# Performance work log

Measured on AMD Instinct MI355X. Metric: run time of the kernel, lower is better.

## Reference

```python
import jax, jax.numpy as jnp
import numpy as np

HEADS = 16
LN_EPS = 1e-5


def setup_inputs() -> dict:
    key = jax.random.key(0)
    ks = jax.random.split(key, 4)
    B, S, C, U = 2, 2048, 1024, 1024
    scale = 1.0 / np.sqrt(C)
    return {
        "inputs": jax.random.normal(ks[0], (B, S, C), dtype=jnp.float32),
        "Wq": jax.random.normal(ks[1], (C, U), dtype=jnp.float32) * scale,
        "bq": jnp.zeros((U,), dtype=jnp.float32),
        "Wk": jax.random.normal(ks[2], (C, U), dtype=jnp.float32) * scale,
        "bk": jnp.zeros((U,), dtype=jnp.float32),
        "Wv": jax.random.normal(ks[3], (C, U), dtype=jnp.float32) * scale,
        "bv": jnp.zeros((U,), dtype=jnp.float32),
        "ln_gamma": jnp.ones((S, U), dtype=jnp.float32),
        "ln_beta": jnp.zeros((S, U), dtype=jnp.float32),
    }


def reference(inputs, Wq, bq, Wk, bk, Wv, bv, ln_gamma, ln_beta):
    B, S, C = inputs.shape
    U = Wq.shape[1]
    H = HEADS
    dh = U // H

    Q = inputs @ Wq + bq  # [B,S,U]
    K = inputs @ Wk + bk
    V = inputs @ Wv + bv

    # torch: concat(split(X, U//H, dim=-1), dim=0) -> head-major stacking on batch
    def split_heads(X):
        return jnp.moveaxis(X.reshape(B, S, H, dh), 2, 0).reshape(H * B, S, dh)

    Q_, K_, V_ = split_heads(Q), split_heads(K), split_heads(V)

    scores = jnp.einsum('bqd,bkd->bqk', Q_, K_) / jnp.sqrt(jnp.float32(dh))
    tri = jnp.tril(jnp.ones((S, S), dtype=bool))  # causal mask
    scores = jnp.where(tri[None, :, :], scores, jnp.float32(-1e9))
    attn = jax.nn.softmax(scores, axis=-1)
    out_ = jnp.einsum('bqk,bkd->bqd', attn, V_)  # [H*B,S,dh]

    # inverse: split on batch into H chunks of size B, concat on feature dim
    out = jnp.moveaxis(out_.reshape(H, B, S, dh), 0, 2).reshape(B, S, U)

    out = out + inputs  # residual

    # LayerNorm over normalized_shape=[S, U] (joint seq+feature stats)
    mu = jnp.mean(out, axis=(-2, -1), keepdims=True)
    var = jnp.mean(jnp.square(out - mu), axis=(-2, -1), keepdims=True)
    out = (out - mu) / jnp.sqrt(var + LN_EPS) * ln_gamma + ln_beta
    return out
```

## Files before the change

### kernel.cpp

```cpp
#include <hip/hip_runtime.h>
#include <hip/hip_bf16.h>


typedef __bf16 bf16_t;
typedef __bf16 bf16x8 __attribute__((ext_vector_type(8)));
typedef __bf16 bf16x4 __attribute__((ext_vector_type(4)));
typedef _Float16 f16_t;
typedef _Float16 f16x2 __attribute__((ext_vector_type(2)));
typedef _Float16 f16x4 __attribute__((ext_vector_type(4)));
typedef _Float16 f16x8 __attribute__((ext_vector_type(8)));
typedef float f32x4 __attribute__((ext_vector_type(4)));

constexpr int Bsz = 2;
constexpr int Seq = 2048;
constexpr int Cdim = 1024;
constexpr int Udim = 1024;
constexpr int Hn = 16;
constexpr int Dh = 64;
constexpr int Mrows = Bsz * Seq;
constexpr int PerBatch = Seq * Udim;
constexpr float SCLQ = 0.125f * 1.44269504088896340736f;

__device__ __forceinline__ void gload16(const void* g, void* l)
{
    __builtin_amdgcn_global_load_lds(
        (const __attribute__((address_space(1))) void*)g,
        (__attribute__((address_space(3))) void*)l, 16, 0, 0);
}

__device__ __forceinline__ f16x2 pkrtz(float a, float b)
{
    return __builtin_bit_cast(f16x2, __builtin_amdgcn_cvt_pkrtz(a, b));
}

__global__ __launch_bounds__(256)
void prep(const float* __restrict__ X,
          const float* __restrict__ Wq, const float* __restrict__ Wk,
          const float* __restrict__ Wv,
          bf16_t* __restrict__ Xb,
          bf16_t* __restrict__ Tq, bf16_t* __restrict__ Tk,
          bf16_t* __restrict__ Tv, float* __restrict__ stats)
{
    int z = blockIdx.z;
    int tid = threadIdx.x;
    if (z < 3) {
        const float* W = (z == 0) ? Wq : (z == 1) ? Wk : Wv;
        bf16_t* T = (z == 0) ? Tq : (z == 1) ? Tk : Tv;
        __shared__ bf16_t t[64][65];
        int x0 = blockIdx.x * 64, y0 = blockIdx.y * 64;
        int tx = tid & 63, ty = tid >> 6;
        for (int i = ty; i < 64; i += 4)
            t[i][tx] = (bf16_t)W[(size_t)(y0 + i) * Cdim + x0 + tx];
        __syncthreads();
        for (int i = ty; i < 64; i += 4)
            T[(size_t)(x0 + i) * Cdim + y0 + tx] = t[tx][i];
    } else {
        int bi = blockIdx.y * 16 + blockIdx.x;
        if (bi == 0 && tid < 4) stats[tid] = 0.0f;
        const float4* Xv = (const float4*)X;
#pragma unroll
        for (int k = 0; k < 16; k++) {
            int i = bi * 4096 + k * 256 + tid;
            float4 v = Xv[i];
            bf16x4 o = { (bf16_t)v.x, (bf16_t)v.y, (bf16_t)v.z, (bf16_t)v.w };
            *(bf16x4*)(Xb + (size_t)i * 4) = o;
        }
    }
}

__global__ __launch_bounds__(256)
void gemm_qkv(const bf16_t* __restrict__ X,
              const bf16_t* __restrict__ Wt0, const bf16_t* __restrict__ Wt1,
              const bf16_t* __restrict__ Wt2,
              const float* __restrict__ b0, const float* __restrict__ b1,
              const float* __restrict__ b2,
              f16_t* __restrict__ O0, f16_t* __restrict__ O1, f16_t* __restrict__ O2v)
{
    int z = blockIdx.z;
    const bf16_t* Wt = (z == 0) ? Wt0 : (z == 1) ? Wt1 : Wt2;
    const float* bias = (z == 0) ? b0 : (z == 1) ? b1 : b2;
    float scl = (z == 0) ? SCLQ : 1.0f;

    constexpr int Kd = 1024, Nd = 1024;
    __shared__ __align__(16) bf16_t As[128 * 32];
    __shared__ __align__(16) bf16_t Bs[128 * 32];

    int tid = threadIdx.x;
    int wave = tid >> 6, lane = tid & 63, quad = lane >> 4, l16 = lane & 15;
    int wm = (wave & 1) * 64, wn = (wave >> 1) * 64;
    int m0 = blockIdx.y * 128, n0 = blockIdx.x * 128;

    f32x4 acc[4][4] = {};

    int e0 = wave * 512 + lane * 8;
    int r0 = e0 >> 5, c0 = e0 & 31;
    int e1 = e0 + 2048;
    int r1 = e1 >> 5, c1 = e1 & 31;
    const bf16_t* Ag = X + (size_t)m0 * Kd;
    const bf16_t* Bg = Wt + (size_t)n0 * Kd;
    bf16_t* AsW0 = As + wave * 512;
    bf16_t* AsW1 = As + 2048 + wave * 512;
    bf16_t* BsW0 = Bs + wave * 512;
    bf16_t* BsW1 = Bs + 2048 + wave * 512;

    for (int k0 = 0; k0 < Kd; k0 += 32) {
        gload16(Ag + (size_t)r0 * Kd + k0 + c0, AsW0);
        gload16(Ag + (size_t)r1 * Kd + k0 + c1, AsW1);
        gload16(Bg + (size_t)r0 * Kd + k0 + c0, BsW0);
        gload16(Bg + (size_t)r1 * Kd + k0 + c1, BsW1);
        __syncthreads();

        bf16x8 af[4], bfr[4];
#pragma unroll
        for (int i = 0; i < 4; i++)
            af[i] = *(const bf16x8*)&As[(wm + i * 16 + l16) * 32 + quad * 8];
#pragma unroll
        for (int i = 0; i < 4; i++)
            bfr[i] = *(const bf16x8*)&Bs[(wn + i * 16 + l16) * 32 + quad * 8];
#pragma unroll
        for (int mt = 0; mt < 4; mt++)
#pragma unroll
            for (int nt = 0; nt < 4; nt++)
                acc[mt][nt] = __builtin_amdgcn_mfma_f32_16x16x32_bf16(
                    af[mt], bfr[nt], acc[mt][nt], 0, 0, 0);
        __syncthreads();
    }

    if (z < 2) {
        f16_t* Og = (z == 0) ? O0 : O1;
#pragma unroll
        for (int nt = 0; nt < 4; nt++) {
            int col = n0 + wn + nt * 16 + l16;
            float bv = bias[col];
#pragma unroll
            for (int mt = 0; mt < 4; mt++) {
                int row = m0 + wm + mt * 16 + quad * 4;
#pragma unroll
                for (int r = 0; r < 4; r++)
                    Og[(size_t)(row + r) * Nd + col] = (f16_t)((acc[mt][nt][r] + bv) * scl);
            }
        }
    } else {
        int bb = m0 >> 11;
#pragma unroll
        for (int nt = 0; nt < 4; nt++) {
            int col = n0 + wn + nt * 16 + l16;
            float bv = bias[col];
            int h = col >> 6, d = col & 63;
            f16_t* vbase = O2v + (((size_t)(bb * Hn + h) * Dh + d) << 11);
#pragma unroll
            for (int mt = 0; mt < 4; mt++) {
                int row = m0 + wm + mt * 16 + quad * 4;
                int s = row & (Seq - 1);
                f16x4 pk;
#pragma unroll
                for (int r = 0; r < 4; r++) pk[r] = (f16_t)(acc[mt][nt][r] + bv);
                *(f16x4*)(vbase + s) = pk;
            }
        }
    }
}

__global__ __launch_bounds__(256)
void attn7(const f16_t* __restrict__ Q, const f16_t* __restrict__ K,
           const f16_t* __restrict__ Vt, const float* __restrict__ X,
           bf16_t* __restrict__ R, float* __restrict__ stats)
{
    int id = blockIdx.x;
    int c = id & 7;
    int r8 = id >> 3;
    int g = r8 & 3;
    int kk = r8 >> 2;
    int bh = (g << 3) | c;
    int b = bh >> 4, h = bh & 15;
    int qtile = 31 - kk;

    int tid = threadIdx.x;
    int w = tid >> 6, lane = tid & 63, quad = lane >> 4, l16 = lane & 15;
    size_t bS = (size_t)b * Seq;

    __shared__ f16_t Ks[2][64][72];
    __shared__ f16_t Vs[2][64][72];

    const f16_t* Kg = K + bS * Udim + h * Dh;
    const f16_t* Vg = Vt + ((size_t)(b * Hn + h)) * Dh * Seq;

    int sr = tid >> 2, sc = (tid & 3) * 16;
    int q0 = qtile * 64 + w * 16;
    int qidx = q0 + l16;

    const f16_t* Qp = Q + (bS + qidx) * Udim + h * Dh;
    f16x8 qf[2];
#pragma unroll
    for (int s = 0; s < 2; s++) qf[s] = *(const f16x8*)(Qp + s * 32 + quad * 8);

    f32x4 Oacc[4] = {};
    float lsum = 0.0f;

    const f16_t* kp = Kg + (size_t)sr * Udim + sc;
    const f16_t* vp = Vg + (size_t)sr * Seq + sc;

    {
        f16x8 k0 = *(const f16x8*)kp;
        f16x8 k1 = *(const f16x8*)(kp + 8);
        f16x8 v0 = *(const f16x8*)vp;
        f16x8 v1 = *(const f16x8*)(vp + 8);
        *(f16x8*)&Ks[0][sr][sc] = k0;
        *(f16x8*)&Ks[0][sr][sc + 8] = k1;
        *(f16x8*)&Vs[0][sr][sc] = v0;
        *(f16x8*)&Vs[0][sr][sc + 8] = v1;
        kp += (size_t)64 * Udim;
        vp += 64;
    }
    __syncthreads();

    int buf = 0;
    for (int i = 0; i < qtile; i++) {
        f16x8 nk0 = *(const f16x8*)kp;
        f16x8 nk1 = *(const f16x8*)(kp + 8);
        f16x8 nv0 = *(const f16x8*)vp;
        f16x8 nv1 = *(const f16x8*)(vp + 8);
        kp += (size_t)64 * Udim;
        vp += 64;

        f32x4 st[4];
#pragma unroll
        for (int t = 0; t < 4; t++) {
            f32x4 a = {};
#pragma unroll
            for (int s = 0; s < 2; s++) {
                f16x8 kf = *(const f16x8*)&Ks[buf][t * 16 + l16][s * 32 + quad * 8];
                a = __builtin_amdgcn_mfma_f32_16x16x32_f16(kf, qf[s], a, 0, 0, 0);
            }
            st[t] = a;
        }

        f16x4 pf[4];
#pragma unroll
        for (int t = 0; t < 4; t++) {
            float p0 = exp2f(st[t][0]);
            float p1 = exp2f(st[t][1]);
            float p2 = exp2f(st[t][2]);
            float p3 = exp2f(st[t][3]);
            lsum += (p0 + p1) + (p2 + p3);
            f16x2 lo = pkrtz(p0, p1);
            f16x2 hi = pkrtz(p2, p3);
            pf[t][0] = lo[0]; pf[t][1] = lo[1];
            pf[t][2] = hi[0]; pf[t][3] = hi[1];
        }

#pragma unroll
        for (int t = 0; t < 4; t++)
#pragma unroll
            for (int dt = 0; dt < 4; dt++) {
                f16x4 vf = *(const f16x4*)&Vs[buf][dt * 16 + l16][t * 16 + quad * 4];
                Oacc[dt] = __builtin_amdgcn_mfma_f32_16x16x16f16(vf, pf[t], Oacc[dt], 0, 0, 0);
            }

        *(f16x8*)&Ks[buf ^ 1][sr][sc] = nk0;
        *(f16x8*)&Ks[buf ^ 1][sr][sc + 8] = nk1;
        *(f16x8*)&Vs[buf ^ 1][sr][sc] = nv0;
        *(f16x8*)&Vs[buf ^ 1][sr][sc + 8] = nv1;
        __syncthreads();
        buf ^= 1;
    }

    {
        int kv0 = qtile * 64;
#pragma unroll
        for (int t = 0; t < 4; t++) {
            if (t <= w) {
                f32x4 a = {};
#pragma unroll
                for (int s = 0; s < 2; s++) {
                    f16x8 kf = *(const f16x8*)&Ks[buf][t * 16 + l16][s * 32 + quad * 8];
                    a = __builtin_amdgcn_mfma_f32_16x16x32_f16(kf, qf[s], a, 0, 0, 0);
                }
                f16x4 pfd;
#pragma unroll
                for (int r = 0; r < 4; r++) {
                    float sv = a[r];
                    if (kv0 + t * 16 + quad * 4 + r > qidx) sv = -1e30f;
                    float pv = exp2f(sv);
                    lsum += pv;
                    pfd[r] = (f16_t)pv;
                }
#pragma unroll
                for (int dt = 0; dt < 4; dt++) {
                    f16x4 vf = *(const f16x4*)&Vs[buf][dt * 16 + l16][t * 16 + quad * 4];
                    Oacc[dt] = __builtin_amdgcn_mfma_f32_16x16x16f16(vf, pfd, Oacc[dt], 0, 0, 0);
                }
            }
        }
    }

    lsum += __shfl_xor(lsum, 16);
    lsum += __shfl_xor(lsum, 32);
    float invl = 1.0f / lsum;

    float s_acc = 0.0f, ss_acc = 0.0f;
    const float* Xp = X + (bS + qidx) * Udim + h * Dh;
    bf16_t* Rp = R + (bS + qidx) * Udim + h * Dh;
#pragma unroll
    for (int dt = 0; dt < 4; dt++) {
        f32x4 xv = *(const f32x4*)(Xp + dt * 16 + quad * 4);
        f32x4 o = Oacc[dt] * invl + xv;
        bf16x4 ob;
#pragma unroll
        for (int r = 0; r < 4; r++) {
            ob[r] = (bf16_t)o[r];
            s_acc += o[r];
            ss_acc += o[r] * o[r];
        }
        *(bf16x4*)(Rp + dt * 16 + quad * 4) = ob;
    }

#pragma unroll
    for (int o = 1; o < 64; o <<= 1) {
        s_acc += __shfl_xor(s_acc, o);
        ss_acc += __shfl_xor(ss_acc, o);
    }
    __shared__ float red[8];
    if (lane == 0) { red[w] = s_acc; red[4 + w] = ss_acc; }
    __syncthreads();
    if (tid == 0) {
        atomicAdd(&stats[b], red[0] + red[1] + red[2] + red[3]);
        atomicAdd(&stats[2 + b], red[4] + red[5] + red[6] + red[7]);
    }
}

__global__ __launch_bounds__(256)
void ln_norm(const bf16_t* __restrict__ R, const float* __restrict__ gamma,
             const float* __restrict__ beta, const float* __restrict__ stats,
             float* __restrict__ out)
{
    constexpr float invN = 1.0f / (float)PerBatch;
    float mu[2], inv[2];
#pragma unroll
    for (int b = 0; b < 2; b++) {
        float m = stats[b] * invN;
        float var = stats[2 + b] * invN - m * m;
        mu[b] = m;
        inv[b] = rsqrtf(var + 1e-5f);
    }
    int i = blockIdx.x * 256 + threadIdx.x;
    int f = i * 8;
    int b = f >> 21;
    int su = f & (PerBatch - 1);
    bf16x8 rv = *(const bf16x8*)(R + f);
    float4 g0 = *(const float4*)(gamma + su);
    float4 g1 = *(const float4*)(gamma + su + 4);
    float4 be0 = *(const float4*)(beta + su);
    float4 be1 = *(const float4*)(beta + su + 4);
    float4 o0, o1;
    o0.x = ((float)rv[0] - mu[b]) * inv[b] * g0.x + be0.x;
    o0.y = ((float)rv[1] - mu[b]) * inv[b] * g0.y + be0.y;
    o0.z = ((float)rv[2] - mu[b]) * inv[b] * g0.z + be0.z;
    o0.w = ((float)rv[3] - mu[b]) * inv[b] * g0.w + be0.w;
    o1.x = ((float)rv[4] - mu[b]) * inv[b] * g1.x + be1.x;
    o1.y = ((float)rv[5] - mu[b]) * inv[b] * g1.y + be1.y;
    o1.z = ((float)rv[6] - mu[b]) * inv[b] * g1.z + be1.z;
    o1.w = ((float)rv[7] - mu[b]) * inv[b] * g1.w + be1.w;
    *(float4*)(out + f) = o0;
    *(float4*)(out + f + 4) = o1;
}

extern "C" void kernel_launch(void* const* d_in, const int* in_sizes, int n_in,
                              void* d_out, int out_size, void* d_ws, size_t ws_size,
                              hipStream_t stream)
{
    const float* X     = (const float*)d_in[0];
    const float* Wq    = (const float*)d_in[1];
    const float* bq    = (const float*)d_in[2];
    const float* Wk    = (const float*)d_in[3];
    const float* bk    = (const float*)d_in[4];
    const float* Wv    = (const float*)d_in[5];
    const float* bv    = (const float*)d_in[6];
    const float* gamma = (const float*)d_in[7];
    const float* beta  = (const float*)d_in[8];
    float* out = (float*)d_out;

    char* ws = (char*)d_ws;
    size_t off = 0;
    auto alloc = [&](size_t bytes) -> void* {
        void* p = ws + off;
        off += (bytes + 255) & ~(size_t)255;
        return p;
    };
    bf16_t* Xb = (bf16_t*)alloc((size_t)Mrows * Cdim * 2);
    bf16_t* Tq = (bf16_t*)alloc((size_t)Cdim * Udim * 2);
    bf16_t* Tk = (bf16_t*)alloc((size_t)Cdim * Udim * 2);
    bf16_t* Tv = (bf16_t*)alloc((size_t)Cdim * Udim * 2);
    f16_t*  Qb = (f16_t*)alloc((size_t)Mrows * Udim * 2);
    f16_t*  Kb = (f16_t*)alloc((size_t)Mrows * Udim * 2);
    f16_t*  Vtb = (f16_t*)alloc((size_t)Mrows * Udim * 2);
    bf16_t* Rb = (bf16_t*)alloc((size_t)Mrows * Udim * 2);
    float*  stats = (float*)alloc(4 * sizeof(float));

    prep<<<dim3(16, 16, 4), 256, 0, stream>>>(X, Wq, Wk, Wv, Xb, Tq, Tk, Tv, stats);
    gemm_qkv<<<dim3(8, 32, 3), 256, 0, stream>>>(Xb, Tq, Tk, Tv, bq, bk, bv, Qb, Kb, Vtb);
    attn7<<<dim3(1024), 256, 0, stream>>>(Qb, Kb, Vtb, X, Rb, stats);
    ln_norm<<<dim3(2048), 256, 0, stream>>>(Rb, gamma, beta, stats, out);
}
```

Baseline: 187.8 us.

## Pair complementary causal query tiles per block to balance work and share K/V

Each attention block now handles two query tiles, p and 31-p, so every block does the same amount of causal work, and each K/V tile staged in shared memory serves both query tiles. The grid is halved to 512 blocks. This targets the load imbalance of triangular causal attention and redundant K/V loads. In exchange, register pressure rises from two accumulator sets, which may lower occupancy, and there are fewer blocks to fill the GPU.

```diff
diff --git a/kernel.cpp b/kernel.cpp
--- a/kernel.cpp
+++ b/kernel.cpp
@@ -162,7 +162,7 @@
 }
 
 __global__ __launch_bounds__(256)
-void attn7(const f16_t* __restrict__ Q, const f16_t* __restrict__ K,
+void attn8(const f16_t* __restrict__ Q, const f16_t* __restrict__ K,
            const f16_t* __restrict__ Vt, const float* __restrict__ X,
            bf16_t* __restrict__ R, float* __restrict__ stats)
 {
@@ -170,10 +170,10 @@
     int c = id & 7;
     int r8 = id >> 3;
     int g = r8 & 3;
-    int kk = r8 >> 2;
+    int p = r8 >> 2;
     int bh = (g << 3) | c;
     int b = bh >> 4, h = bh & 15;
-    int qtile = 31 - kk;
+    int pA = p, pB = 31 - p;
 
     int tid = threadIdx.x;
     int w = tid >> 6, lane = tid & 63, quad = lane >> 4, l16 = lane & 15;
@@ -186,16 +186,22 @@
     const f16_t* Vg = Vt + ((size_t)(b * Hn + h)) * Dh * Seq;
 
     int sr = tid >> 2, sc = (tid & 3) * 16;
-    int q0 = qtile * 64 + w * 16;
-    int qidx = q0 + l16;
-
-    const f16_t* Qp = Q + (bS + qidx) * Udim + h * Dh;
-    f16x8 qf[2];
-#pragma unroll
-    for (int s = 0; s < 2; s++) qf[s] = *(const f16x8*)(Qp + s * 32 + quad * 8);
-
-    f32x4 Oacc[4] = {};
-    float lsum = 0.0f;
+    int qA = pA * 64 + w * 16 + l16;
+    int qB = pB * 64 + w * 16 + l16;
+
+    f16x8 qfA[2], qfB[2];
+    {
+        const f16_t* QpA = Q + (bS + qA) * Udim + h * Dh;
+        const f16_t* QpB = Q + (bS + qB) * Udim + h * Dh;
+#pragma unroll
+        for (int s = 0; s < 2; s++) {
+            qfA[s] = *(const f16x8*)(QpA + s * 32 + quad * 8);
+            qfB[s] = *(const f16x8*)(QpB + s * 32 + quad * 8);
+        }
+    }
+
+    f32x4 OA[4] = {}, OB[4] = {};
+    float lsA = 0.0f, lsB = 0.0f;
 
     const f16_t* kp = Kg + (size_t)sr * Udim + sc;
     const f16_t* vp = Vg + (size_t)sr * Seq + sc;
@@ -215,7 +221,7 @@
     __syncthreads();
 
     int buf = 0;
-    for (int i = 0; i < qtile; i++) {
+    for (int i = 0; i < pB; i++) {
         f16x8 nk0 = *(const f16x8*)kp;
         f16x8 nk1 = *(const f16x8*)(kp + 8);
         f16x8 nv0 = *(const f16x8*)vp;
@@ -223,39 +229,95 @@
         kp += (size_t)64 * Udim;
         vp += 64;
 
-        f32x4 st[4];
+        bool aFull = (i < pA);
+        bool aDiag = (i == pA);
+
+        f16x4 pfB[4];
+        {
+            f32x4 stB[4];
+#pragma unroll
+            for (int t = 0; t < 4; t++) {
+                f32x4 a = {};
+#pragma unroll
+                for (int s = 0; s < 2; s++) {
+                    f16x8 kf = *(const f16x8*)&Ks[buf][t * 16 + l16][s * 32 + quad * 8];
+                    a = __builtin_amdgcn_mfma_f32_16x16x32_f16(kf, qfB[s], a, 0, 0, 0);
+                }
+                stB[t] = a;
+            }
+#pragma unroll
+            for (int t = 0; t < 4; t++) {
+                float p0 = exp2f(stB[t][0]);
+                float p1 = exp2f(stB[t][1]);
+                float p2 = exp2f(stB[t][2]);
+                float p3 = exp2f(stB[t][3]);
+                lsB += (p0 + p1) + (p2 + p3);
+                f16x2 lo = pkrtz(p0, p1);
+                f16x2 hi = pkrtz(p2, p3);
+                pfB[t][0] = lo[0]; pfB[t][1] = lo[1];
+                pfB[t][2] = hi[0]; pfB[t][3] = hi[1];
+            }
+        }
+
+        f16x4 pfA[4];
+        if (aFull) {
+            f32x4 stA[4];
+#pragma unroll
+            for (int t = 0; t < 4; t++) {
+                f32x4 a = {};
+#pragma unroll
+                for (int s = 0; s < 2; s++) {
+                    f16x8 kf = *(const f16x8*)&Ks[buf][t * 16 + l16][s * 32 + quad * 8];
+                    a = __builtin_amdgcn_mfma_f32_16x16x32_f16(kf, qfA[s], a, 0, 0, 0);
+                }
+                stA[t] = a;
+            }
+#pragma unroll
+            for (int t = 0; t < 4; t++) {
+                float p0 = exp2f(stA[t][0]);
+                float p1 = exp2f(stA[t][1]);
+                float p2 = exp2f(stA[t][2]);
+                float p3 = exp2f(stA[t][3]);
+                lsA += (p0 + p1) + (p2 + p3);
+                f16x2 lo = pkrtz(p0, p1);
+                f16x2 hi = pkrtz(p2, p3);
+                pfA[t][0] = lo[0]; pfA[t][1] = lo[1];
+                pfA[t][2] = hi[0]; pfA[t][3] = hi[1];
+            }
+        } else if (aDiag) {
+            int kv0 = i * 64;
+#pragma unroll
+            for (int t = 0; t < 4; t++) {
+                if (t <= w) {
+                    f32x4 a = {};
+#pragma unroll
+                    for (int s = 0; s < 2; s++) {
+                        f16x8 kf = *(const f16x8*)&Ks[buf][t * 16 + l16][s * 32 + quad * 8];
+                        a = __builtin_amdgcn_mfma_f32_16x16x32_f16(kf, qfA[s], a, 0, 0, 0);
+                    }
+#pragma unroll
+                    for (int r = 0; r < 4; r++) {
+                        float sv = a[r];
+                        if (kv0 + t * 16 + quad * 4 + r > qA) sv = -1e30f;
+                        float pv = exp2f(sv);
+                        lsA += pv;
+                        pfA[t][r] = (f16_t)pv;
+                    }
+                }
+            }
+        }
+
 #pragma unroll
         for (int t = 0; t < 4; t++) {
-            f32x4 a = {};
-#pragma unroll
-            for (int s = 0; s < 2; s++) {
-                f16x8 kf = *(const f16x8*)&Ks[buf][t * 16 + l16][s * 32 + quad * 8];
-                a = __builtin_amdgcn_mfma_f32_16x16x32_f16(kf, qf[s], a, 0, 0, 0);
-            }
-            st[t] = a;
-        }
-
-        f16x4 pf[4];
-#pragma unroll
-        for (int t = 0; t < 4; t++) {
-            float p0 = exp2f(st[t][0]);
-            float p1 = exp2f(st[t][1]);
-            float p2 = exp2f(st[t][2]);
-            float p3 = exp2f(st[t][3]);
-            lsum += (p0 + p1) + (p2 + p3);
-            f16x2 lo = pkrtz(p0, p1);
-            f16x2 hi = pkrtz(p2, p3);
-            pf[t][0] = lo[0]; pf[t][1] = lo[1];
-            pf[t][2] = hi[0]; pf[t][3] = hi[1];
-        }
-
-#pragma unroll
-        for (int t = 0; t < 4; t++)
+            bool aUse = aFull || (aDiag && t <= w);
 #pragma unroll
             for (int dt = 0; dt < 4; dt++) {
                 f16x4 vf = *(const f16x4*)&Vs[buf][dt * 16 + l16][t * 16 + quad * 4];
-                Oacc[dt] = __builtin_amdgcn_mfma_f32_16x16x16f16(vf, pf[t], Oacc[dt], 0, 0, 0);
-            }
+                OB[dt] = __builtin_amdgcn_mfma_f32_16x16x16f16(vf, pfB[t], OB[dt], 0, 0, 0);
+                if (aUse)
+                    OA[dt] = __builtin_amdgcn_mfma_f32_16x16x16f16(vf, pfA[t], OA[dt], 0, 0, 0);
+            }
+        }
 
         *(f16x8*)&Ks[buf ^ 1][sr][sc] = nk0;
         *(f16x8*)&Ks[buf ^ 1][sr][sc + 8] = nk1;
@@ -266,7 +328,7 @@
     }
 
     {
-        int kv0 = qtile * 64;
+        int kv0 = pB * 64;
 #pragma unroll
         for (int t = 0; t < 4; t++) {
             if (t <= w) {
@@ -274,45 +336,56 @@
 #pragma unroll
                 for (int s = 0; s < 2; s++) {
                     f16x8 kf = *(const f16x8*)&Ks[buf][t * 16 + l16][s * 32 + quad * 8];
-                    a = __builtin_amdgcn_mfma_f32_16x16x32_f16(kf, qf[s], a, 0, 0, 0);
+                    a = __builtin_amdgcn_mfma_f32_16x16x32_f16(kf, qfB[s], a, 0, 0, 0);
                 }
                 f16x4 pfd;
 #pragma unroll
                 for (int r = 0; r < 4; r++) {
                     float sv = a[r];
-                    if (kv0 + t * 16 + quad * 4 + r > qidx) sv = -1e30f;
+                    if (kv0 + t * 16 + quad * 4 + r > qB) sv = -1e30f;
                     float pv = exp2f(sv);
-                    lsum += pv;
+                    lsB += pv;
                     pfd[r] = (f16_t)pv;
                 }
 #pragma unroll
                 for (int dt = 0; dt < 4; dt++) {
                     f16x4 vf = *(const f16x4*)&Vs[buf][dt * 16 + l16][t * 16 + quad * 4];
-                    Oacc[dt] = __builtin_amdgcn_mfma_f32_16x16x16f16(vf, pfd, Oacc[dt], 0, 0, 0);
-                }
-            }
-        }
-    }
-
-    lsum += __shfl_xor(lsum, 16);
-    lsum += __shfl_xor(lsum, 32);
-    float invl = 1.0f / lsum;
+                    OB[dt] = __builtin_amdgcn_mfma_f32_16x16x16f16(vf, pfd, OB[dt], 0, 0, 0);
+                }
+            }
+        }
+    }
+
+    lsA += __shfl_xor(lsA, 16);
+    lsA += __shfl_xor(lsA, 32);
+    lsB += __shfl_xor(lsB, 16);
+    lsB += __shfl_xor(lsB, 32);
+    float invA = 1.0f / lsA;
+    float invB = 1.0f / lsB;
 
     float s_acc = 0.0f, ss_acc = 0.0f;
-    const float* Xp = X + (bS + qidx) * Udim + h * Dh;
-    bf16_t* Rp = R + (bS + qidx) * Udim + h * Dh;
-#pragma unroll
-    for (int dt = 0; dt < 4; dt++) {
-        f32x4 xv = *(const f32x4*)(Xp + dt * 16 + quad * 4);
-        f32x4 o = Oacc[dt] * invl + xv;
-        bf16x4 ob;
-#pragma unroll
-        for (int r = 0; r < 4; r++) {
-            ob[r] = (bf16_t)o[r];
-            s_acc += o[r];
-            ss_acc += o[r] * o[r];
-        }
-        *(bf16x4*)(Rp + dt * 16 + quad * 4) = ob;
+    {
+        const float* XpA = X + (bS + qA) * Udim + h * Dh;
+        bf16_t* RpA = R + (bS + qA) * Udim + h * Dh;
+        const float* XpB = X + (bS + qB) * Udim + h * Dh;
+        bf16_t* RpB = R + (bS + qB) * Udim + h * Dh;
+#pragma unroll
+        for (int dt = 0; dt < 4; dt++) {
+            f32x4 xa = *(const f32x4*)(XpA + dt * 16 + quad * 4);
+            f32x4 oa = OA[dt] * invA + xa;
+            f32x4 xb = *(const f32x4*)(XpB + dt * 16 + quad * 4);
+            f32x4 ob = OB[dt] * invB + xb;
+            bf16x4 pa, pb;
+#pragma unroll
+            for (int r = 0; r < 4; r++) {
+                pa[r] = (bf16_t)oa[r];
+                pb[r] = (bf16_t)ob[r];
+                s_acc += oa[r] + ob[r];
+                ss_acc += oa[r] * oa[r] + ob[r] * ob[r];
+            }
+            *(bf16x4*)(RpA + dt * 16 + quad * 4) = pa;
+            *(bf16x4*)(RpB + dt * 16 + quad * 4) = pb;
+        }
     }
 
 #pragma unroll
@@ -399,6 +472,6 @@
 
     prep<<<dim3(16, 16, 4), 256, 0, stream>>>(X, Wq, Wk, Wv, Xb, Tq, Tk, Tv, stats);
     gemm_qkv<<<dim3(8, 32, 3), 256, 0, stream>>>(Xb, Tq, Tk, Tv, bq, bk, bv, Qb, Kb, Vtb);
-    attn7<<<dim3(1024), 256, 0, stream>>>(Qb, Kb, Vtb, X, Rb, stats);
+    attn8<<<dim3(512), 256, 0, stream>>>(Qb, Kb, Vtb, X, Rb, stats);
     ln_norm<<<dim3(2048), 256, 0, stream>>>(Rb, gamma, beta, stats, out);
 }
```

New measurement: 204.4 us. 1.09x slower.

## Fuse attention and LayerNorm via cooperative grid sync, rebalance q-tile order

Applied to the files above, without the earlier changes.

Attention and the final LayerNorm are merged into one cooperative kernel. Each block keeps its output tile in registers, adds its partial sums to global stats atomically, waits on a grid-wide sync, then normalizes and writes the fp32 output directly. This removes the bf16 intermediate write/read and the separate ln_norm launch. The block-to-q-tile mapping also changes to interleave light and heavy causal tiles. The cost is that all 1024 blocks must be co-resident (launch_bounds with 4 blocks per CU), and the grid sync adds a barrier; if the cooperative launch fails, the code falls back to the old two-kernel path.

```diff
diff --git a/kernel.cpp b/kernel.cpp
--- a/kernel.cpp
+++ b/kernel.cpp
@@ -1,6 +1,9 @@
 #include <hip/hip_runtime.h>
 #include <hip/hip_bf16.h>
-
+#include <hip/hip_cooperative_groups.h>
+
+
+namespace cg = cooperative_groups;
 
 typedef __bf16 bf16_t;
 typedef __bf16 bf16x8 __attribute__((ext_vector_type(8)));
@@ -161,27 +164,18 @@
     }
 }
 
-__global__ __launch_bounds__(256)
-void attn7(const f16_t* __restrict__ Q, const f16_t* __restrict__ K,
-           const f16_t* __restrict__ Vt, const float* __restrict__ X,
-           bf16_t* __restrict__ R, float* __restrict__ stats)
-{
-    int id = blockIdx.x;
-    int c = id & 7;
-    int r8 = id >> 3;
-    int g = r8 & 3;
-    int kk = r8 >> 2;
-    int bh = (g << 3) | c;
-    int b = bh >> 4, h = bh & 15;
-    int qtile = 31 - kk;
-
-    int tid = threadIdx.x;
+struct AttnCore {
+    f32x4 Oacc[4];
+    float lsum;
+};
+
+__device__ __forceinline__ void attn_core(
+    const f16_t* __restrict__ Q, const f16_t* __restrict__ K,
+    const f16_t* __restrict__ Vt, int b, int h, int qtile,
+    int tid, f16_t Ks[2][64][72], f16_t Vs[2][64][72], AttnCore& out_)
+{
     int w = tid >> 6, lane = tid & 63, quad = lane >> 4, l16 = lane & 15;
     size_t bS = (size_t)b * Seq;
-
-    __shared__ f16_t Ks[2][64][72];
-    __shared__ f16_t Vs[2][64][72];
-
     const f16_t* Kg = K + bS * Udim + h * Dh;
     const f16_t* Vg = Vt + ((size_t)(b * Hn + h)) * Dh * Seq;
 
@@ -296,7 +290,115 @@
 
     lsum += __shfl_xor(lsum, 16);
     lsum += __shfl_xor(lsum, 32);
-    float invl = 1.0f / lsum;
+#pragma unroll
+    for (int dt = 0; dt < 4; dt++) out_.Oacc[dt] = Oacc[dt];
+    out_.lsum = lsum;
+}
+
+__device__ __forceinline__ void map_block(int id, int& b, int& h, int& qtile)
+{
+    int c = id & 7;
+    int r8 = id >> 3;
+    int g = r8 & 3;
+    int kk = r8 >> 2;
+    int bh = (g << 3) | c;
+    b = bh >> 4; h = bh & 15;
+    int j = kk & 7, qt4 = kk >> 3;
+    qtile = (qt4 == 0) ? j : (qt4 == 1) ? (31 - j)
+          : (qt4 == 2) ? (8 + j) : (23 - j);
+}
+
+__global__ __launch_bounds__(256, 4)
+void attn9(const f16_t* __restrict__ Q, const f16_t* __restrict__ K,
+           const f16_t* __restrict__ Vt, const float* __restrict__ X,
+           const float* __restrict__ gamma, const float* __restrict__ beta,
+           float* __restrict__ out, float* __restrict__ stats)
+{
+    __shared__ f16_t Ks[2][64][72];
+    __shared__ f16_t Vs[2][64][72];
+    int b, h, qtile;
+    map_block(blockIdx.x, b, h, qtile);
+    int tid = threadIdx.x;
+    int w = tid >> 6, lane = tid & 63, quad = lane >> 4, l16 = lane & 15;
+    size_t bS = (size_t)b * Seq;
+    int qidx = qtile * 64 + w * 16 + l16;
+
+    AttnCore acr;
+    attn_core(Q, K, Vt, b, h, qtile, tid, Ks, Vs, acr);
+    float invl = 1.0f / acr.lsum;
+
+    float s_acc = 0.0f, ss_acc = 0.0f;
+    const float* Xp = X + (bS + qidx) * Udim + h * Dh;
+#pragma unroll
+    for (int dt = 0; dt < 4; dt++) {
+        f32x4 xv = *(const f32x4*)(Xp + dt * 16 + quad * 4);
+        f32x4 o = acr.Oacc[dt] * invl + xv;
+        acr.Oacc[dt] = o;
+#pragma unroll
+        for (int r = 0; r < 4; r++) {
+            s_acc += o[r];
+            ss_acc += o[r] * o[r];
+        }
+    }
+
+#pragma unroll
+    for (int o = 1; o < 64; o <<= 1) {
+        s_acc += __shfl_xor(s_acc, o);
+        ss_acc += __shfl_xor(ss_acc, o);
+    }
+    __shared__ float red[8];
+    if (lane == 0) { red[w] = s_acc; red[4 + w] = ss_acc; }
+    __syncthreads();
+    if (tid == 0) {
+        atomicAdd(&stats[b], red[0] + red[1] + red[2] + red[3]);
+        atomicAdd(&stats[2 + b], red[4] + red[5] + red[6] + red[7]);
+    }
+
+    cg::this_grid().sync();
+
+    __shared__ float mi[2];
+    if (tid == 0) {
+        constexpr float invN = 1.0f / (float)PerBatch;
+        float sb  = __hip_atomic_load(&stats[b], __ATOMIC_RELAXED,
+                                      __HIP_MEMORY_SCOPE_AGENT);
+        float ssb = __hip_atomic_load(&stats[2 + b], __ATOMIC_RELAXED,
+                                      __HIP_MEMORY_SCOPE_AGENT);
+        float m = sb * invN;
+        mi[0] = m;
+        mi[1] = rsqrtf(ssb * invN - m * m + 1e-5f);
+    }
+    __syncthreads();
+    float mu = mi[0], inv = mi[1];
+
+    const float* Gp = gamma + (size_t)qidx * Udim + h * Dh;
+    const float* Bp = beta + (size_t)qidx * Udim + h * Dh;
+    float* Op = out + (bS + qidx) * Udim + h * Dh;
+#pragma unroll
+    for (int dt = 0; dt < 4; dt++) {
+        f32x4 gv = *(const f32x4*)(Gp + dt * 16 + quad * 4);
+        f32x4 bv = *(const f32x4*)(Bp + dt * 16 + quad * 4);
+        f32x4 o = (acr.Oacc[dt] - mu) * inv * gv + bv;
+        *(f32x4*)(Op + dt * 16 + quad * 4) = o;
+    }
+}
+
+__global__ __launch_bounds__(256)
+void attn7f(const f16_t* __restrict__ Q, const f16_t* __restrict__ K,
+            const f16_t* __restrict__ Vt, const float* __restrict__ X,
+            bf16_t* __restrict__ R, float* __restrict__ stats)
+{
+    __shared__ f16_t Ks[2][64][72];
+    __shared__ f16_t Vs[2][64][72];
+    int b, h, qtile;
+    map_block(blockIdx.x, b, h, qtile);
+    int tid = threadIdx.x;
+    int w = tid >> 6, lane = tid & 63, quad = lane >> 4, l16 = lane & 15;
+    size_t bS = (size_t)b * Seq;
+    int qidx = qtile * 64 + w * 16 + l16;
+
+    AttnCore acr;
+    attn_core(Q, K, Vt, b, h, qtile, tid, Ks, Vs, acr);
+    float invl = 1.0f / acr.lsum;
 
     float s_acc = 0.0f, ss_acc = 0.0f;
     const float* Xp = X + (bS + qidx) * Udim + h * Dh;
@@ -304,7 +406,7 @@
 #pragma unroll
     for (int dt = 0; dt < 4; dt++) {
         f32x4 xv = *(const f32x4*)(Xp + dt * 16 + quad * 4);
-        f32x4 o = Oacc[dt] * invl + xv;
+        f32x4 o = acr.Oacc[dt] * invl + xv;
         bf16x4 ob;
 #pragma unroll
         for (int r = 0; r < 4; r++) {
@@ -399,6 +501,14 @@
 
     prep<<<dim3(16, 16, 4), 256, 0, stream>>>(X, Wq, Wk, Wv, Xb, Tq, Tk, Tv, stats);
     gemm_qkv<<<dim3(8, 32, 3), 256, 0, stream>>>(Xb, Tq, Tk, Tv, bq, bk, bv, Qb, Kb, Vtb);
-    attn7<<<dim3(1024), 256, 0, stream>>>(Qb, Kb, Vtb, X, Rb, stats);
-    ln_norm<<<dim3(2048), 256, 0, stream>>>(Rb, gamma, beta, stats, out);
-}
+
+    void* kargs[] = { (void*)&Qb, (void*)&Kb, (void*)&Vtb, (void*)&X,
+                      (void*)&gamma, (void*)&beta, (void*)&out, (void*)&stats };
+    hipError_t cerr = hipLaunchCooperativeKernel((const void*)attn9, dim3(1024),
+                                                 dim3(256), kargs, 0, stream);
+    if (cerr != hipSuccess) {
+        (void)hipGetLastError();
+        attn7f<<<dim3(1024), 256, 0, stream>>>(Qb, Kb, Vtb, X, Rb, stats);
+        ln_norm<<<dim3(2048), 256, 0, stream>>>(Rb, gamma, beta, stats, out);
+    }
+}
```

Result: slower. 341.0 us (+81.6%).
